# Kernel tuning notes

Hardware: AMD Instinct MI355X
Metric: run time of the kernel (lower is better)

Reference implementation:

```python
import jax, jax.numpy as jnp
import numpy as np

B, N, VF, EF, DV, DE, LN = 64, 64, 32, 16, 128, 128, 4
EPS_INNER = 128.0  # BatchNorm1d(MAX_N, internal_d_vert): 2nd positional arg is eps (faithful to source bug)
EPS_BN = 1e-5


def gev_layer(v_in, e_in, evW, evb, eW, eb, vW, vb, relu=True):
    act = jax.nn.relu if relu else (lambda x: x)
    ev = v_in @ evW + evb                                   # [B,N,De]
    # outer_v_sum: ev.unsqueeze(1) + ev.unsqueeze(2) -> [B,N,N,De]
    e_out = act(e_in @ eW + eb + ev[:, None, :, :] + ev[:, :, None, :])
    per_v_e = e_out.sum(axis=1)                             # sum-aggregate over dim 1
    v_out = act(jnp.concatenate([per_v_e, v_in], axis=-1) @ vW + vb)
    return v_out, e_out


def bn_flat(v, g, b):
    # BatchNorm1d(N*VF) on [B, N*VF] in training mode (biased var)
    x = v.reshape(-1, N * VF)
    mu = x.mean(axis=0)
    var = x.var(axis=0)
    x = (x - mu) * jax.lax.rsqrt(var + EPS_BN) * g + b
    return x.reshape(-1, N, VF)


def bn_inner(v, g, b):
    # BatchNorm1d(MAX_N, eps=128) on [B, N, D]: channels are the N axis, stats over (B, D)
    mu = v.mean(axis=(0, 2), keepdims=True)
    var = v.var(axis=(0, 2), keepdims=True)
    return (v - mu) * jax.lax.rsqrt(var + EPS_INNER) * g[None, :, None] + b[None, :, None]


def setup_inputs() -> dict:
    key = jax.random.key(0)
    ks = jax.random.split(key, 24)
    s = 0.01  # force_lin_init with init_noise=0.01, biases zero
    nrm = lambda k, shp: jax.random.normal(k, shp, dtype=jnp.float32) * s
    inp = {
        "v": jax.random.normal(ks[0], (B, N, VF), dtype=jnp.float32),
        "e": jax.random.normal(ks[1], (B, N, N, EF), dtype=jnp.float32),
        "bn_in_g": jnp.ones((N * VF,), jnp.float32),
        "bn_in_b": jnp.zeros((N * VF,), jnp.float32),
        "g1_evW": nrm(ks[2], (VF, DE)), "g1_evb": jnp.zeros((DE,), jnp.float32),
        "g1_eW": nrm(ks[3], (EF, DE)), "g1_eb": jnp.zeros((DE,), jnp.float32),
        "g1_vW": nrm(ks[4], (VF + DE, DV)), "g1_vb": jnp.zeros((DV,), jnp.float32),
        "inn_evW": nrm(ks[5], (LN, DV, DE)), "inn_evb": jnp.zeros((LN, DE), jnp.float32),
        "inn_eW": nrm(ks[6], (LN, DE, DE)), "inn_eb": jnp.zeros((LN, DE), jnp.float32),
        "inn_vW": nrm(ks[7], (LN, DV + DE, DV)), "inn_vb": jnp.zeros((LN, DV), jnp.float32),
        "bn_g": jnp.ones((LN, N), jnp.float32),
        "bn_b": jnp.zeros((LN, N), jnp.float32),
        "g3_evW": nrm(ks[8], (DV, 1)), "g3_evb": jnp.zeros((1,), jnp.float32),
        "g3_eW": nrm(ks[9], (DE, 1)), "g3_eb": jnp.zeros((1,), jnp.float32),
        "g3_vW": nrm(ks[10], (DV + 1, 1)), "g3_vb": jnp.zeros((1,), jnp.float32),
    }
    return inp


def reference(v, e, bn_in_g, bn_in_b, g1_evW, g1_evb, g1_eW, g1_eb, g1_vW, g1_vb,
              inn_evW, inn_evb, inn_eW, inn_eb, inn_vW, inn_vb, bn_g, bn_b,
              g3_evW, g3_evb, g3_eW, g3_eb, g3_vW, g3_vb):
    v = bn_flat(v, bn_in_g, bn_in_b)
    v, e = gev_layer(v, e, g1_evW, g1_evb, g1_eW, g1_eb, g1_vW, g1_vb)
    for i in range(LN):
        v_next, e_next = gev_layer(v, e, inn_evW[i], inn_evb[i], inn_eW[i], inn_eb[i], inn_vW[i], inn_vb[i])
        v = v_next + v  # resnet
        e = e_next + e
        v = bn_inner(v, bn_g[i], bn_b[i])
    v, e = gev_layer(v, e, g3_evW, g3_evb, g3_eW, g3_eb, g3_vW, g3_vb, relu=False)
    return v, e
```

## Files before the change

### kernel.cpp

```cpp
#include <hip/hip_runtime.h>
#include <hip/hip_bf16.h>


typedef __bf16 bf16_t;
typedef __bf16 bf16x8 __attribute__((ext_vector_type(8)));
typedef __bf16 bf16x4 __attribute__((ext_vector_type(4)));
typedef float f32x4 __attribute__((ext_vector_type(4)));

__device__ __forceinline__ void bar_lgkm() {
  asm volatile("s_waitcnt lgkmcnt(0)\n\ts_barrier" ::: "memory");
}

__global__ __launch_bounds__(256) void k_prep(const float* __restrict__ vin,
    const float* __restrict__ g, const float* __restrict__ bt,
    const float* __restrict__ eW, float* __restrict__ v0,
    bf16_t* __restrict__ Wt, float* __restrict__ stats) {
  __shared__ float red[8][32][2];
  __shared__ float scb[32], shb[32];
  const int blk = blockIdx.x, tid = threadIdx.x;
  if (blk < 64) {
    const int chq = tid & 31, bq = tid >> 5;
    const int ch = blk * 32 + chq;
    float s = 0.f, s2 = 0.f;
#pragma unroll
    for (int t = 0; t < 8; ++t) {
      float x = vin[(bq * 8 + t) * 2048 + ch];
      s += x; s2 += x * x;
    }
    red[bq][chq][0] = s;
    red[bq][chq][1] = s2;
    __syncthreads();
    if (tid < 32) {
      float S = 0.f, S2 = 0.f;
#pragma unroll
      for (int q = 0; q < 8; ++q) { S += red[q][tid][0]; S2 += red[q][tid][1]; }
      float mu = S * (1.f / 64.f);
      float var = S2 * (1.f / 64.f) - mu * mu;
      float sc = rsqrtf(var + 1e-5f) * g[blk * 32 + tid];
      scb[tid] = sc;
      shb[tid] = bt[blk * 32 + tid] - mu * sc;
    }
    __syncthreads();
    const float sc = scb[chq], sh = shb[chq];
#pragma unroll
    for (int t = 0; t < 8; ++t) {
      int b = bq * 8 + t;
      v0[b * 2048 + ch] = vin[b * 2048 + ch] * sc + sh;
    }
  } else if (blk < 320) {
    int idx = (blk - 64) * 256 + tid;
    int l = idx >> 14, r = idx & 16383, n = r >> 7, k = r & 127;
    Wt[idx] = (bf16_t)eW[(l << 14) + (k << 7) + n];
  } else {
    for (int i = tid; i < 512; i += 256) stats[i] = 0.f;
  }
}

template <int K>
__global__ __launch_bounds__(256) void k_ev(const float* __restrict__ v_in,
    const float* __restrict__ W, const float* __restrict__ bias,
    float* __restrict__ out) {
  __shared__ float rows_s[8][K];
  const int r0 = blockIdx.x * 8;
  const int tid = threadIdx.x;
  const int c = tid & 127, h = tid >> 7;
  for (int idx = tid; idx < 8 * K; idx += 256) {
    int rr = idx / K, kk = idx % K;
    rows_s[rr][kk] = v_in[(r0 + rr) * K + kk];
  }
  __syncthreads();
  float acc[4];
  const float bv = bias[c];
#pragma unroll
  for (int r = 0; r < 4; ++r) acc[r] = bv;
  for (int k4 = 0; k4 < K; k4 += 4) {
    float w0 = W[(k4 + 0) * 128 + c], w1 = W[(k4 + 1) * 128 + c];
    float w2 = W[(k4 + 2) * 128 + c], w3 = W[(k4 + 3) * 128 + c];
#pragma unroll
    for (int r = 0; r < 4; ++r) {
      float4 x = *(const float4*)&rows_s[h * 4 + r][k4];
      acc[r] += x.x * w0 + x.y * w1 + x.z * w2 + x.w * w3;
    }
  }
#pragma unroll
  for (int r = 0; r < 4; ++r) out[(r0 + h * 4 + r) * 128 + c] = acc[r];
}

__global__ __launch_bounds__(256) void k_evbn(float* __restrict__ v,
    const float* __restrict__ stats, const float* __restrict__ g,
    const float* __restrict__ bt, const float* __restrict__ W,
    const float* __restrict__ bias, float* __restrict__ out) {
  __shared__ float rows_s[8][128];
  const int r0 = blockIdx.x * 8;
  const int tid = threadIdx.x;
  const int c = tid & 127, h = tid >> 7;
#pragma unroll
  for (int u = 0; u < 4; ++u) {
    int idx = u * 256 + tid;
    int rr = idx >> 7, k = idx & 127;
    int n = (r0 + rr) & 63;
    float mu = stats[n] * (1.f / 8192.f);
    float var = stats[64 + n] * (1.f / 8192.f) - mu * mu;
    float sc = rsqrtf(var + 128.f) * g[n];
    float x = (v[(r0 + rr) * 128 + k] - mu) * sc + bt[n];
    rows_s[rr][k] = x;
    v[(r0 + rr) * 128 + k] = x;
  }
  __syncthreads();
  float acc[4];
  const float bv = bias[c];
#pragma unroll
  for (int r = 0; r < 4; ++r) acc[r] = bv;
  for (int k4 = 0; k4 < 128; k4 += 4) {
    float w0 = W[(k4 + 0) * 128 + c], w1 = W[(k4 + 1) * 128 + c];
    float w2 = W[(k4 + 2) * 128 + c], w3 = W[(k4 + 3) * 128 + c];
#pragma unroll
    for (int r = 0; r < 4; ++r) {
      float4 x = *(const float4*)&rows_s[h * 4 + r][k4];
      acc[r] += x.x * w0 + x.y * w1 + x.z * w2 + x.w * w3;
    }
  }
#pragma unroll
  for (int r = 0; r < 4; ++r) out[(r0 + h * 4 + r) * 128 + c] = acc[r];
}

__global__ __launch_bounds__(256) void k_edge_g1(const float* __restrict__ e0,
    const float* __restrict__ eW, const float* __restrict__ eb,
    const float* __restrict__ ev, bf16_t* __restrict__ e_ws,
    float* __restrict__ pve) {
  __shared__ bf16_t A0s[2][64][40];
  __shared__ bf16_t Os[2][64][136];
  const int b = blockIdx.x >> 5, j0 = (blockIdx.x & 31) * 2;
  const int tid = threadIdx.x;
  const int lane = tid & 63, w = tid >> 6;
  const int quad = lane >> 4, l16 = lane & 15;
#pragma unroll
  for (int t = 0; t < 2; ++t) {
    int idx = tid + t * 256;
    int row = idx >> 3, off = (idx & 7) * 4;
    int jc = off >> 4, k = off & 15;
    f32x4 x = *(const f32x4*)&e0[((b * 64 + row) * 64 + j0) * 16 + off];
    bf16x4 y;
#pragma unroll
    for (int r = 0; r < 4; ++r) y[r] = (bf16_t)x[r];
    *(bf16x4*)&A0s[jc][row][k] = y;
    bf16x4 z = {(bf16_t)0.f, (bf16_t)0.f, (bf16_t)0.f, (bf16_t)0.f};
    *(bf16x4*)&A0s[jc][row][16 + k] = z;
  }
  const int c0[2] = {w * 32 + quad * 4, w * 32 + 16 + quad * 4};
  bf16x8 wf[2];
#pragma unroll
  for (int nt = 0; nt < 2; ++nt) {
    const int c = w * 32 + nt * 16 + l16;
#pragma unroll
    for (int jj = 0; jj < 8; ++jj)
      wf[nt][jj] = (quad < 2) ? (bf16_t)eW[(quad * 8 + jj) * 128 + c] : (bf16_t)0.f;
  }
  f32x4 acc[2][4][2];
  {
    f32x4 ebv[2], evj[2][2], evi[4][2];
#pragma unroll
    for (int nt = 0; nt < 2; ++nt) {
      ebv[nt] = *(const f32x4*)&eb[c0[nt]];
#pragma unroll
      for (int jc = 0; jc < 2; ++jc)
        evj[jc][nt] = *(const f32x4*)&ev[(b * 64 + j0 + jc) * 128 + c0[nt]];
#pragma unroll
      for (int mt = 0; mt < 4; ++mt)
        evi[mt][nt] = *(const f32x4*)&ev[(b * 64 + mt * 16 + l16) * 128 + c0[nt]];
    }
#pragma unroll
    for (int jc = 0; jc < 2; ++jc)
#pragma unroll
      for (int mt = 0; mt < 4; ++mt)
#pragma unroll
        for (int nt = 0; nt < 2; ++nt)
          acc[jc][mt][nt] = ebv[nt] + evj[jc][nt] + evi[mt][nt];
  }
  __syncthreads();
#pragma unroll
  for (int jc = 0; jc < 2; ++jc) {
#pragma unroll
    for (int mt = 0; mt < 4; ++mt) {
      bf16x8 ef = *(const bf16x8*)&A0s[jc][mt * 16 + l16][quad * 8];
#pragma unroll
      for (int nt = 0; nt < 2; ++nt)
        acc[jc][mt][nt] = __builtin_amdgcn_mfma_f32_16x16x32_bf16(wf[nt], ef, acc[jc][mt][nt], 0, 0, 0);
    }
  }
#pragma unroll
  for (int jc = 0; jc < 2; ++jc) {
#pragma unroll
    for (int nt = 0; nt < 2; ++nt) {
      f32x4 ps = {0.f, 0.f, 0.f, 0.f};
#pragma unroll
      for (int mt = 0; mt < 4; ++mt) {
        const int i = mt * 16 + l16;
        bf16x4 outv;
#pragma unroll
        for (int r = 0; r < 4; ++r) {
          float vv = fmaxf(acc[jc][mt][nt][r], 0.f);
          ps[r] += vv;
          outv[r] = (bf16_t)vv;
        }
        *(bf16x4*)&Os[jc][i][c0[nt]] = outv;
      }
#pragma unroll
      for (int m = 1; m <= 8; m <<= 1) {
#pragma unroll
        for (int r = 0; r < 4; ++r) ps[r] += __shfl_xor(ps[r], m);
      }
      if (l16 == 0) *(f32x4*)&pve[(b * 64 + j0 + jc) * 128 + c0[nt]] = ps;
    }
  }
  __syncthreads();
  {
    bf16_t* ebase = &e_ws[((size_t)(b * 64 + j0) * 64) * 128];
#pragma unroll
    for (int t = 0; t < 8; ++t) {
      int idx = tid + t * 256;
      *(int4*)&ebase[idx * 8] =
          *(const int4*)&Os[idx >> 10][(idx >> 4) & 63][(idx & 15) * 8];
    }
  }
}

__global__ __launch_bounds__(256) void k_vg1_ev(const float* __restrict__ pve,
    const float* __restrict__ v0, const float* __restrict__ vW,
    const float* __restrict__ vb, const float* __restrict__ evW,
    const float* __restrict__ evb, float* __restrict__ v, float* __restrict__ ev) {
  __shared__ float in_s[8][160];
  __shared__ float vr[8][128];
  const int r0 = blockIdx.x * 8;
  const int tid = threadIdx.x;
  const int c = tid & 127, h = tid >> 7;
#pragma unroll
  for (int u = 0; u < 4; ++u) {
    int idx = u * 256 + tid;
    int rr = idx >> 7, k = idx & 127;
    in_s[rr][k] = pve[(r0 + rr) * 128 + k];
  }
  {
    int rr = tid >> 5, k = tid & 31;
    in_s[rr][128 + k] = v0[(r0 + rr) * 32 + k];
  }
  __syncthreads();
  float acc[4];
  const float bv = vb[c];
#pragma unroll
  for (int r = 0; r < 4; ++r) acc[r] = bv;
  for (int k4 = 0; k4 < 160; k4 += 4) {
    float w0 = vW[(k4 + 0) * 128 + c], w1 = vW[(k4 + 1) * 128 + c];
    float w2 = vW[(k4 + 2) * 128 + c], w3 = vW[(k4 + 3) * 128 + c];
#pragma unroll
    for (int r = 0; r < 4; ++r) {
      float4 x = *(const float4*)&in_s[h * 4 + r][k4];
      acc[r] += x.x * w0 + x.y * w1 + x.z * w2 + x.w * w3;
    }
  }
#pragma unroll
  for (int r = 0; r < 4; ++r) {
    float val = fmaxf(acc[r], 0.f);
    vr[h * 4 + r][c] = val;
    v[(r0 + h * 4 + r) * 128 + c] = val;
  }
  __syncthreads();
  float acc2[4];
  const float bv2 = evb[c];
#pragma unroll
  for (int r = 0; r < 4; ++r) acc2[r] = bv2;
  for (int k4 = 0; k4 < 128; k4 += 4) {
    float w0 = evW[(k4 + 0) * 128 + c], w1 = evW[(k4 + 1) * 128 + c];
    float w2 = evW[(k4 + 2) * 128 + c], w3 = evW[(k4 + 3) * 128 + c];
#pragma unroll
    for (int r = 0; r < 4; ++r) {
      float4 x = *(const float4*)&vr[h * 4 + r][k4];
      acc2[r] += x.x * w0 + x.y * w1 + x.z * w2 + x.w * w3;
    }
  }
#pragma unroll
  for (int r = 0; r < 4; ++r) ev[(r0 + h * 4 + r) * 128 + c] = acc2[r];
}

template <bool LAST>
__global__ __launch_bounds__(256) void k_edge_inner(bf16_t* __restrict__ e_ws,
    const bf16_t* __restrict__ Wt, const float* __restrict__ eb,
    const float* __restrict__ ev, float* __restrict__ pve,
    const float* __restrict__ eW3, float* __restrict__ edt) {
  __shared__ bf16_t As[2][64][136];
  __shared__ float W3s[128];
  const int b = blockIdx.x >> 5, j0 = (blockIdx.x & 31) * 2;
  const int tid = threadIdx.x;
  const int lane = tid & 63, w = tid >> 6;
  const int quad = lane >> 4, l16 = lane & 15;
  bf16_t* ebase = &e_ws[((size_t)(b * 64 + j0) * 64) * 128];
  int4 stg[8];
#pragma unroll
  for (int t = 0; t < 8; ++t) {
    int idx = tid + t * 256;
    stg[t] = *(const int4*)&ebase[idx * 8];
  }
  if (LAST) {
    if (tid < 128) W3s[tid] = eW3[tid];
  }
  bf16x8 wf[2][4];
#pragma unroll
  for (int nt = 0; nt < 2; ++nt)
#pragma unroll
    for (int ks = 0; ks < 4; ++ks)
      wf[nt][ks] = *(const bf16x8*)&Wt[(w * 32 + nt * 16 + l16) * 128 + ks * 32 + quad * 8];
  const int c0[2] = {w * 32 + quad * 4, w * 32 + 16 + quad * 4};
  f32x4 acc[2][4][2];
  {
    f32x4 ebv[2], evj[2][2], evi[4][2];
#pragma unroll
    for (int nt = 0; nt < 2; ++nt) {
      ebv[nt] = *(const f32x4*)&eb[c0[nt]];
#pragma unroll
      for (int jc = 0; jc < 2; ++jc)
        evj[jc][nt] = *(const f32x4*)&ev[(b * 64 + j0 + jc) * 128 + c0[nt]];
#pragma unroll
      for (int mt = 0; mt < 4; ++mt)
        evi[mt][nt] = *(const f32x4*)&ev[(b * 64 + mt * 16 + l16) * 128 + c0[nt]];
    }
#pragma unroll
    for (int jc = 0; jc < 2; ++jc)
#pragma unroll
      for (int mt = 0; mt < 4; ++mt)
#pragma unroll
        for (int nt = 0; nt < 2; ++nt)
          acc[jc][mt][nt] = ebv[nt] + evj[jc][nt] + evi[mt][nt];
  }
#pragma unroll
  for (int t = 0; t < 8; ++t) {
    int idx = tid + t * 256;
    *(int4*)&As[idx >> 10][(idx >> 4) & 63][(idx & 15) * 8] = stg[t];
  }
  bar_lgkm();
#pragma unroll
  for (int ks = 0; ks < 4; ++ks) {
    bf16x8 ef[2][4];
#pragma unroll
    for (int jc = 0; jc < 2; ++jc)
#pragma unroll
      for (int mt = 0; mt < 4; ++mt)
        ef[jc][mt] = *(const bf16x8*)&As[jc][mt * 16 + l16][ks * 32 + quad * 8];
#pragma unroll
    for (int jc = 0; jc < 2; ++jc)
#pragma unroll
      for (int mt = 0; mt < 4; ++mt)
#pragma unroll
        for (int nt = 0; nt < 2; ++nt)
          acc[jc][mt][nt] = __builtin_amdgcn_mfma_f32_16x16x32_bf16(wf[nt][ks], ef[jc][mt], acc[jc][mt][nt], 0, 0, 0);
  }
  if (!LAST) {
#pragma unroll
    for (int jc = 0; jc < 2; ++jc) {
#pragma unroll
      for (int nt = 0; nt < 2; ++nt) {
        f32x4 ps = {0.f, 0.f, 0.f, 0.f};
#pragma unroll
        for (int mt = 0; mt < 4; ++mt) {
          const int i = mt * 16 + l16;
          bf16x4 eo = *(const bf16x4*)&As[jc][i][c0[nt]];
          bf16x4 outv;
#pragma unroll
          for (int r = 0; r < 4; ++r) {
            float vv = fmaxf(acc[jc][mt][nt][r], 0.f);
            ps[r] += vv;
            outv[r] = (bf16_t)(vv + (float)eo[r]);
          }
          *(bf16x4*)&ebase[jc * 8192 + i * 128 + c0[nt]] = outv;
        }
#pragma unroll
        for (int m = 1; m <= 8; m <<= 1) {
#pragma unroll
          for (int r = 0; r < 4; ++r) ps[r] += __shfl_xor(ps[r], m);
        }
        if (l16 == 0) *(f32x4*)&pve[(b * 64 + j0 + jc) * 128 + c0[nt]] = ps;
      }
    }
  } else {
    bar_lgkm();
#pragma unroll
    for (int jc = 0; jc < 2; ++jc) {
#pragma unroll
      for (int nt = 0; nt < 2; ++nt) {
        f32x4 ps = {0.f, 0.f, 0.f, 0.f};
#pragma unroll
        for (int mt = 0; mt < 4; ++mt) {
          const int i = mt * 16 + l16;
          bf16x4 eo = *(const bf16x4*)&As[jc][i][c0[nt]];
          bf16x4 outv;
#pragma unroll
          for (int r = 0; r < 4; ++r) {
            float vv = fmaxf(acc[jc][mt][nt][r], 0.f);
            ps[r] += vv;
            outv[r] = (bf16_t)(vv + (float)eo[r]);
          }
          *(bf16x4*)&As[jc][i][c0[nt]] = outv;
        }
#pragma unroll
        for (int m = 1; m <= 8; m <<= 1) {
#pragma unroll
          for (int r = 0; r < 4; ++r) ps[r] += __shfl_xor(ps[r], m);
        }
        if (l16 == 0) *(f32x4*)&pve[(b * 64 + j0 + jc) * 128 + c0[nt]] = ps;
      }
    }
    bar_lgkm();
    const int i = tid >> 2, q = tid & 3;
#pragma unroll
    for (int jc = 0; jc < 2; ++jc) {
      float d = 0.f;
#pragma unroll
      for (int t = 0; t < 4; ++t) {
        bf16x8 x = *(const bf16x8*)&As[jc][i][q * 32 + t * 8];
#pragma unroll
        for (int u = 0; u < 8; ++u) d += (float)x[u] * W3s[q * 32 + t * 8 + u];
      }
      d += __shfl_xor(d, 1);
      d += __shfl_xor(d, 2);
      if (q == 0) edt[(b * 64 + j0 + jc) * 64 + i] = d;
    }
  }
}

__global__ __launch_bounds__(256) void k_v_inner(const float* __restrict__ pve,
    float* __restrict__ v, const float* __restrict__ vW,
    const float* __restrict__ vb, float* __restrict__ stats) {
  __shared__ float in_s[8][256];
  __shared__ float outs[8][132];
  __shared__ float part[16][2];
  const int r0 = blockIdx.x * 8;
  const int tid = threadIdx.x;
  const int c = tid & 127, h = tid >> 7;
#pragma unroll
  for (int u = 0; u < 4; ++u) {
    int idx = u * 256 + tid;
    int rr = idx >> 7, k = idx & 127;
    in_s[rr][k] = pve[(r0 + rr) * 128 + k];
    in_s[rr][128 + k] = v[(r0 + rr) * 128 + k];
  }
  __syncthreads();
  float acc[4];
  const float bv = vb[c];
#pragma unroll
  for (int r = 0; r < 4; ++r) acc[r] = bv;
  for (int k4 = 0; k4 < 256; k4 += 4) {
    float w0 = vW[(k4 + 0) * 128 + c], w1 = vW[(k4 + 1) * 128 + c];
    float w2 = vW[(k4 + 2) * 128 + c], w3 = vW[(k4 + 3) * 128 + c];
#pragma unroll
    for (int r = 0; r < 4; ++r) {
      float4 x = *(const float4*)&in_s[h * 4 + r][k4];
      acc[r] += x.x * w0 + x.y * w1 + x.z * w2 + x.w * w3;
    }
  }
#pragma unroll
  for (int r = 0; r < 4; ++r) {
    float val = fmaxf(acc[r], 0.f) + in_s[h * 4 + r][128 + c];
    outs[h * 4 + r][c] = val;
    v[(r0 + h * 4 + r) * 128 + c] = val;
  }
  __syncthreads();
  if (tid < 16) {
    int rr = tid >> 1, half = tid & 1;
    float s = 0.f, s2 = 0.f;
    for (int k = 0; k < 64; ++k) {
      float x = outs[rr][half * 64 + k];
      s += x; s2 += x * x;
    }
    part[tid][0] = s;
    part[tid][1] = s2;
  }
  __syncthreads();
  if (tid < 8) {
    int n = (r0 + tid) & 63;
    atomicAdd(&stats[n], part[tid * 2][0] + part[tid * 2 + 1][0]);
    atomicAdd(&stats[64 + n], part[tid * 2][1] + part[tid * 2 + 1][1]);
  }
}

__global__ __launch_bounds__(256) void k_g3(const float* __restrict__ vv,
    const float* __restrict__ stats3, const float* __restrict__ g,
    const float* __restrict__ bt, const float* __restrict__ evW3,
    const float* __restrict__ evb3, const float* __restrict__ eb3,
    const float* __restrict__ edt, const float* __restrict__ vW3,
    const float* __restrict__ vb3, float* __restrict__ out_v,
    float* __restrict__ out_e) {
  __shared__ float vbn[64][132];
  __shared__ float edts[64][68];
  __shared__ float scs[64], shs[64];
  __shared__ float W3e[128];
  __shared__ float vWs[132];
  __shared__ float ev3s[64];
  __shared__ float pj[4][64];
  const int b = blockIdx.x, tid = threadIdx.x;
  if (tid < 64) {
    float mu = stats3[tid] * (1.f / 8192.f);
    float var = stats3[64 + tid] * (1.f / 8192.f) - mu * mu;
    float sc = rsqrtf(var + 128.f) * g[tid];
    scs[tid] = sc;
    shs[tid] = bt[tid] - mu * sc;
  }
  if (tid < 128) W3e[tid] = evW3[tid];
  if (tid < 129) vWs[tid] = vW3[tid];
  __syncthreads();
#pragma unroll
  for (int t = 0; t < 8; ++t) {
    int idx = t * 1024 + tid * 4;
    int row = idx >> 7, cc = idx & 127;
    f32x4 x = *(const f32x4*)&vv[(b * 64 + row) * 128 + cc];
    *(f32x4*)&vbn[row][cc] = x * scs[row] + shs[row];
  }
#pragma unroll
  for (int t = 0; t < 4; ++t) {
    int idx = t * 1024 + tid * 4;
    int j = idx >> 6, i = idx & 63;
    *(f32x4*)&edts[j][i] = *(const f32x4*)&edt[(b * 64 + j) * 64 + i];
  }
  __syncthreads();
  {
    int i = tid >> 2, q = tid & 3;
    float d = 0.f;
#pragma unroll
    for (int u = 0; u < 32; ++u) d += vbn[i][q * 32 + u] * W3e[q * 32 + u];
    d += __shfl_xor(d, 1);
    d += __shfl_xor(d, 2);
    if (q == 0) ev3s[i] = d + evb3[0];
  }
  __syncthreads();
  {
    int q = tid >> 6, j = tid & 63;
    float s = 0.f;
    const float e3 = eb3[0];
    const float evj = ev3s[j];
#pragma unroll
    for (int r = 0; r < 16; ++r) {
      int i = q * 16 + r;
      float val = edts[j][i] + e3 + ev3s[i] + evj;
      out_e[(b * 64 + i) * 64 + j] = val;
      s += val;
    }
    pj[q][j] = s;
  }
  __syncthreads();
  {
    int n = tid >> 2, q = tid & 3;
    float d = 0.f;
#pragma unroll
    for (int u = 0; u < 32; ++u) d += vbn[n][q * 32 + u] * vWs[1 + q * 32 + u];
    d += __shfl_xor(d, 1);
    d += __shfl_xor(d, 2);
    if (q == 0) {
      float p3 = pj[0][n] + pj[1][n] + pj[2][n] + pj[3][n];
      out_v[b * 64 + n] = d + p3 * vWs[0] + vb3[0];
    }
  }
}

extern "C" void kernel_launch(void* const* d_in, const int* in_sizes, int n_in,
                              void* d_out, int out_size, void* d_ws, size_t ws_size,
                              hipStream_t stream) {
  const float* in_v    = (const float*)d_in[0];
  const float* in_e    = (const float*)d_in[1];
  const float* bn_in_g = (const float*)d_in[2];
  const float* bn_in_b = (const float*)d_in[3];
  const float* g1_evW  = (const float*)d_in[4];
  const float* g1_evb  = (const float*)d_in[5];
  const float* g1_eW   = (const float*)d_in[6];
  const float* g1_eb   = (const float*)d_in[7];
  const float* g1_vW   = (const float*)d_in[8];
  const float* g1_vb   = (const float*)d_in[9];
  const float* inn_evW = (const float*)d_in[10];
  const float* inn_evb = (const float*)d_in[11];
  const float* inn_eW  = (const float*)d_in[12];
  const float* inn_eb  = (const float*)d_in[13];
  const float* inn_vW  = (const float*)d_in[14];
  const float* inn_vb  = (const float*)d_in[15];
  const float* bn_g    = (const float*)d_in[16];
  const float* bn_b    = (const float*)d_in[17];
  const float* g3_evW  = (const float*)d_in[18];
  const float* g3_evb  = (const float*)d_in[19];
  const float* g3_eW   = (const float*)d_in[20];
  const float* g3_eb   = (const float*)d_in[21];
  const float* g3_vW   = (const float*)d_in[22];
  const float* g3_vb   = (const float*)d_in[23];

  char* ws = (char*)d_ws;
  bf16_t* e_ws = (bf16_t*)(ws);
  float* v     = (float*)(ws + 67108864);
  float* ev    = (float*)(ws + 69206016);
  float* pve   = (float*)(ws + 71303168);
  float* v0    = (float*)(ws + 73400320);
  bf16_t* Wt   = (bf16_t*)(ws + 73924608);
  float* edt   = (float*)(ws + 74055680);
  float* stats = (float*)(ws + 75104256);

  float* out_v = (float*)d_out;
  float* out_e = (float*)d_out + 4096;

  k_prep<<<321, 256, 0, stream>>>(in_v, bn_in_g, bn_in_b, inn_eW, v0, Wt, stats);

  k_ev<32><<<512, 256, 0, stream>>>(v0, g1_evW, g1_evb, ev);
  k_edge_g1<<<2048, 256, 0, stream>>>(in_e, g1_eW, g1_eb, ev, e_ws, pve);
  k_vg1_ev<<<512, 256, 0, stream>>>(pve, v0, g1_vW, g1_vb, inn_evW, inn_evb, v, ev);

  for (int l = 0; l < 4; ++l) {
    if (l > 0)
      k_evbn<<<512, 256, 0, stream>>>(v, stats + (l - 1) * 128, bn_g + (l - 1) * 64,
                                      bn_b + (l - 1) * 64, inn_evW + l * 16384,
                                      inn_evb + l * 128, ev);
    if (l < 3)
      k_edge_inner<false><<<2048, 256, 0, stream>>>(e_ws, Wt + l * 16384,
          inn_eb + l * 128, ev, pve, g3_eW, edt);
    else
      k_edge_inner<true><<<2048, 256, 0, stream>>>(e_ws, Wt + l * 16384,
          inn_eb + l * 128, ev, pve, g3_eW, edt);
    k_v_inner<<<512, 256, 0, stream>>>(pve, v, inn_vW + l * 32768, inn_vb + l * 128,
                                       stats + l * 128);
  }

  k_g3<<<64, 256, 0, stream>>>(v, stats + 384, bn_g + 192, bn_b + 192,
                               g3_evW, g3_evb, g3_eb, edt, g3_vW, g3_vb,
                               out_v, out_e);
}
```

Measured before the change: 381.6 us.

## Fold inner BatchNorm into edge projection via column sums, drop k_evbn launches

Result: faster. 371.1 us (-2.8%).

```diff
diff --git a/kernel.cpp b/kernel.cpp
--- a/kernel.cpp
+++ b/kernel.cpp
@@ -13,8 +13,9 @@
 
 __global__ __launch_bounds__(256) void k_prep(const float* __restrict__ vin,
     const float* __restrict__ g, const float* __restrict__ bt,
-    const float* __restrict__ eW, float* __restrict__ v0,
-    bf16_t* __restrict__ Wt, float* __restrict__ stats) {
+    const float* __restrict__ eW, const float* __restrict__ evW,
+    float* __restrict__ v0, bf16_t* __restrict__ Wt,
+    float* __restrict__ stats, float* __restrict__ colsum) {
   __shared__ float red[8][32][2];
   __shared__ float scb[32], shb[32];
   const int blk = blockIdx.x, tid = threadIdx.x;
@@ -53,65 +54,34 @@
     Wt[idx] = (bf16_t)eW[(l << 14) + (k << 7) + n];
   } else {
     for (int i = tid; i < 512; i += 256) stats[i] = 0.f;
-  }
-}
-
-template <int K>
-__global__ __launch_bounds__(256) void k_ev(const float* __restrict__ v_in,
+#pragma unroll
+    for (int t = 0; t < 2; ++t) {
+      int idx = tid + t * 256;
+      int l = idx >> 7, c = idx & 127;
+      float s = 0.f;
+      for (int k = 0; k < 128; ++k) s += evW[(l << 14) + (k << 7) + c];
+      colsum[idx] = s;
+    }
+  }
+}
+
+__global__ __launch_bounds__(256) void k_ev32(const float* __restrict__ v_in,
     const float* __restrict__ W, const float* __restrict__ bias,
     float* __restrict__ out) {
-  __shared__ float rows_s[8][K];
+  __shared__ float rows_s[8][32];
   const int r0 = blockIdx.x * 8;
   const int tid = threadIdx.x;
   const int c = tid & 127, h = tid >> 7;
-  for (int idx = tid; idx < 8 * K; idx += 256) {
-    int rr = idx / K, kk = idx % K;
-    rows_s[rr][kk] = v_in[(r0 + rr) * K + kk];
+  {
+    int rr = tid >> 5, kk = tid & 31;
+    rows_s[rr][kk] = v_in[(r0 + rr) * 32 + kk];
   }
   __syncthreads();
   float acc[4];
   const float bv = bias[c];
 #pragma unroll
   for (int r = 0; r < 4; ++r) acc[r] = bv;
-  for (int k4 = 0; k4 < K; k4 += 4) {
-    float w0 = W[(k4 + 0) * 128 + c], w1 = W[(k4 + 1) * 128 + c];
-    float w2 = W[(k4 + 2) * 128 + c], w3 = W[(k4 + 3) * 128 + c];
-#pragma unroll
-    for (int r = 0; r < 4; ++r) {
-      float4 x = *(const float4*)&rows_s[h * 4 + r][k4];
-      acc[r] += x.x * w0 + x.y * w1 + x.z * w2 + x.w * w3;
-    }
-  }
-#pragma unroll
-  for (int r = 0; r < 4; ++r) out[(r0 + h * 4 + r) * 128 + c] = acc[r];
-}
-
-__global__ __launch_bounds__(256) void k_evbn(float* __restrict__ v,
-    const float* __restrict__ stats, const float* __restrict__ g,
-    const float* __restrict__ bt, const float* __restrict__ W,
-    const float* __restrict__ bias, float* __restrict__ out) {
-  __shared__ float rows_s[8][128];
-  const int r0 = blockIdx.x * 8;
-  const int tid = threadIdx.x;
-  const int c = tid & 127, h = tid >> 7;
-#pragma unroll
-  for (int u = 0; u < 4; ++u) {
-    int idx = u * 256 + tid;
-    int rr = idx >> 7, k = idx & 127;
-    int n = (r0 + rr) & 63;
-    float mu = stats[n] * (1.f / 8192.f);
-    float var = stats[64 + n] * (1.f / 8192.f) - mu * mu;
-    float sc = rsqrtf(var + 128.f) * g[n];
-    float x = (v[(r0 + rr) * 128 + k] - mu) * sc + bt[n];
-    rows_s[rr][k] = x;
-    v[(r0 + rr) * 128 + k] = x;
-  }
-  __syncthreads();
-  float acc[4];
-  const float bv = bias[c];
-#pragma unroll
-  for (int r = 0; r < 4; ++r) acc[r] = bv;
-  for (int k4 = 0; k4 < 128; k4 += 4) {
+  for (int k4 = 0; k4 < 32; k4 += 4) {
     float w0 = W[(k4 + 0) * 128 + c], w1 = W[(k4 + 1) * 128 + c];
     float w2 = W[(k4 + 2) * 128 + c], w3 = W[(k4 + 3) * 128 + c];
 #pragma unroll
@@ -228,7 +198,7 @@
 __global__ __launch_bounds__(256) void k_vg1_ev(const float* __restrict__ pve,
     const float* __restrict__ v0, const float* __restrict__ vW,
     const float* __restrict__ vb, const float* __restrict__ evW,
-    const float* __restrict__ evb, float* __restrict__ v, float* __restrict__ ev) {
+    float* __restrict__ v, float* __restrict__ ev) {
   __shared__ float in_s[8][160];
   __shared__ float vr[8][128];
   const int r0 = blockIdx.x * 8;
@@ -265,10 +235,7 @@
     v[(r0 + h * 4 + r) * 128 + c] = val;
   }
   __syncthreads();
-  float acc2[4];
-  const float bv2 = evb[c];
-#pragma unroll
-  for (int r = 0; r < 4; ++r) acc2[r] = bv2;
+  float acc2[4] = {0.f, 0.f, 0.f, 0.f};
   for (int k4 = 0; k4 < 128; k4 += 4) {
     float w0 = evW[(k4 + 0) * 128 + c], w1 = evW[(k4 + 1) * 128 + c];
     float w2 = evW[(k4 + 2) * 128 + c], w3 = evW[(k4 + 3) * 128 + c];
@@ -285,15 +252,31 @@
 template <bool LAST>
 __global__ __launch_bounds__(256) void k_edge_inner(bf16_t* __restrict__ e_ws,
     const bf16_t* __restrict__ Wt, const float* __restrict__ eb,
-    const float* __restrict__ ev, float* __restrict__ pve,
-    const float* __restrict__ eW3, float* __restrict__ edt) {
+    const float* __restrict__ evb, const float* __restrict__ rawev,
+    const float* __restrict__ colsum, const float* __restrict__ stats_prev,
+    const float* __restrict__ g_prev, const float* __restrict__ bt_prev,
+    float* __restrict__ pve, const float* __restrict__ eW3,
+    float* __restrict__ edt) {
   __shared__ bf16_t As[2][64][136];
   __shared__ float W3s[128];
+  __shared__ float scs[64], shs[64];
   const int b = blockIdx.x >> 5, j0 = (blockIdx.x & 31) * 2;
   const int tid = threadIdx.x;
   const int lane = tid & 63, w = tid >> 6;
   const int quad = lane >> 4, l16 = lane & 15;
   bf16_t* ebase = &e_ws[((size_t)(b * 64 + j0) * 64) * 128];
+  if (tid < 64) {
+    if (stats_prev) {
+      float mu = stats_prev[tid] * (1.f / 8192.f);
+      float var = stats_prev[64 + tid] * (1.f / 8192.f) - mu * mu;
+      float sc = rsqrtf(var + 128.f) * g_prev[tid];
+      scs[tid] = sc;
+      shs[tid] = bt_prev[tid] - mu * sc;
+    } else {
+      scs[tid] = 1.f;
+      shs[tid] = 0.f;
+    }
+  }
   int4 stg[8];
 #pragma unroll
   for (int t = 0; t < 8; ++t) {
@@ -310,26 +293,19 @@
     for (int ks = 0; ks < 4; ++ks)
       wf[nt][ks] = *(const bf16x8*)&Wt[(w * 32 + nt * 16 + l16) * 128 + ks * 32 + quad * 8];
   const int c0[2] = {w * 32 + quad * 4, w * 32 + 16 + quad * 4};
-  f32x4 acc[2][4][2];
-  {
-    f32x4 ebv[2], evj[2][2], evi[4][2];
-#pragma unroll
-    for (int nt = 0; nt < 2; ++nt) {
-      ebv[nt] = *(const f32x4*)&eb[c0[nt]];
-#pragma unroll
-      for (int jc = 0; jc < 2; ++jc)
-        evj[jc][nt] = *(const f32x4*)&ev[(b * 64 + j0 + jc) * 128 + c0[nt]];
-#pragma unroll
-      for (int mt = 0; mt < 4; ++mt)
-        evi[mt][nt] = *(const f32x4*)&ev[(b * 64 + mt * 16 + l16) * 128 + c0[nt]];
-    }
+  f32x4 basev[2], cs[2], evj[2][2], evi[4][2];
+#pragma unroll
+  for (int nt = 0; nt < 2; ++nt) {
+    f32x4 e1 = *(const f32x4*)&eb[c0[nt]];
+    f32x4 e2 = *(const f32x4*)&evb[c0[nt]];
+    basev[nt] = e1 + 2.f * e2;
+    cs[nt] = *(const f32x4*)&colsum[c0[nt]];
 #pragma unroll
     for (int jc = 0; jc < 2; ++jc)
-#pragma unroll
-      for (int mt = 0; mt < 4; ++mt)
-#pragma unroll
-        for (int nt = 0; nt < 2; ++nt)
-          acc[jc][mt][nt] = ebv[nt] + evj[jc][nt] + evi[mt][nt];
+      evj[jc][nt] = *(const f32x4*)&rawev[(b * 64 + j0 + jc) * 128 + c0[nt]];
+#pragma unroll
+    for (int mt = 0; mt < 4; ++mt)
+      evi[mt][nt] = *(const f32x4*)&rawev[(b * 64 + mt * 16 + l16) * 128 + c0[nt]];
   }
 #pragma unroll
   for (int t = 0; t < 8; ++t) {
@@ -337,6 +313,24 @@
     *(int4*)&As[idx >> 10][(idx >> 4) & 63][(idx & 15) * 8] = stg[t];
   }
   bar_lgkm();
+  f32x4 acc[2][4][2];
+  {
+    float scj[2], shj[2];
+#pragma unroll
+    for (int jc = 0; jc < 2; ++jc) { scj[jc] = scs[j0 + jc]; shj[jc] = shs[j0 + jc]; }
+#pragma unroll
+    for (int mt = 0; mt < 4; ++mt) {
+      const int i = mt * 16 + l16;
+      const float sci = scs[i], shi = shs[i];
+#pragma unroll
+      for (int jc = 0; jc < 2; ++jc) {
+        const float shsum = shi + shj[jc];
+#pragma unroll
+        for (int nt = 0; nt < 2; ++nt)
+          acc[jc][mt][nt] = basev[nt] + shsum * cs[nt] + scj[jc] * evj[jc][nt] + sci * evi[mt][nt];
+      }
+    }
+  }
 #pragma unroll
   for (int ks = 0; ks < 4; ++ks) {
     bf16x8 ef[2][4];
@@ -353,62 +347,42 @@
         for (int nt = 0; nt < 2; ++nt)
           acc[jc][mt][nt] = __builtin_amdgcn_mfma_f32_16x16x32_bf16(wf[nt][ks], ef[jc][mt], acc[jc][mt][nt], 0, 0, 0);
   }
+  bar_lgkm();
+#pragma unroll
+  for (int jc = 0; jc < 2; ++jc) {
+#pragma unroll
+    for (int nt = 0; nt < 2; ++nt) {
+      f32x4 ps = {0.f, 0.f, 0.f, 0.f};
+#pragma unroll
+      for (int mt = 0; mt < 4; ++mt) {
+        const int i = mt * 16 + l16;
+        bf16x4 eo = *(const bf16x4*)&As[jc][i][c0[nt]];
+        bf16x4 outv;
+#pragma unroll
+        for (int r = 0; r < 4; ++r) {
+          float vv = fmaxf(acc[jc][mt][nt][r], 0.f);
+          ps[r] += vv;
+          outv[r] = (bf16_t)(vv + (float)eo[r]);
+        }
+        *(bf16x4*)&As[jc][i][c0[nt]] = outv;
+      }
+#pragma unroll
+      for (int m = 1; m <= 8; m <<= 1) {
+#pragma unroll
+        for (int r = 0; r < 4; ++r) ps[r] += __shfl_xor(ps[r], m);
+      }
+      if (l16 == 0) *(f32x4*)&pve[(b * 64 + j0 + jc) * 128 + c0[nt]] = ps;
+    }
+  }
+  bar_lgkm();
   if (!LAST) {
 #pragma unroll
-    for (int jc = 0; jc < 2; ++jc) {
-#pragma unroll
-      for (int nt = 0; nt < 2; ++nt) {
-        f32x4 ps = {0.f, 0.f, 0.f, 0.f};
-#pragma unroll
-        for (int mt = 0; mt < 4; ++mt) {
-          const int i = mt * 16 + l16;
-          bf16x4 eo = *(const bf16x4*)&As[jc][i][c0[nt]];
-          bf16x4 outv;
-#pragma unroll
-          for (int r = 0; r < 4; ++r) {
-            float vv = fmaxf(acc[jc][mt][nt][r], 0.f);
-            ps[r] += vv;
-            outv[r] = (bf16_t)(vv + (float)eo[r]);
-          }
-          *(bf16x4*)&ebase[jc * 8192 + i * 128 + c0[nt]] = outv;
-        }
-#pragma unroll
-        for (int m = 1; m <= 8; m <<= 1) {
-#pragma unroll
-          for (int r = 0; r < 4; ++r) ps[r] += __shfl_xor(ps[r], m);
-        }
-        if (l16 == 0) *(f32x4*)&pve[(b * 64 + j0 + jc) * 128 + c0[nt]] = ps;
-      }
+    for (int t = 0; t < 8; ++t) {
+      int idx = tid + t * 256;
+      *(int4*)&ebase[idx * 8] =
+          *(const int4*)&As[idx >> 10][(idx >> 4) & 63][(idx & 15) * 8];
     }
   } else {
-    bar_lgkm();
-#pragma unroll
-    for (int jc = 0; jc < 2; ++jc) {
-#pragma unroll
-      for (int nt = 0; nt < 2; ++nt) {
-        f32x4 ps = {0.f, 0.f, 0.f, 0.f};
-#pragma unroll
-        for (int mt = 0; mt < 4; ++mt) {
-          const int i = mt * 16 + l16;
-          bf16x4 eo = *(const bf16x4*)&As[jc][i][c0[nt]];
-          bf16x4 outv;
-#pragma unroll
-          for (int r = 0; r < 4; ++r) {
-            float vv = fmaxf(acc[jc][mt][nt][r], 0.f);
-            ps[r] += vv;
-            outv[r] = (bf16_t)(vv + (float)eo[r]);
-          }
-          *(bf16x4*)&As[jc][i][c0[nt]] = outv;
-        }
-#pragma unroll
-        for (int m = 1; m <= 8; m <<= 1) {
-#pragma unroll
-          for (int r = 0; r < 4; ++r) ps[r] += __shfl_xor(ps[r], m);
-        }
-        if (l16 == 0) *(f32x4*)&pve[(b * 64 + j0 + jc) * 128 + c0[nt]] = ps;
-      }
-    }
-    bar_lgkm();
     const int i = tid >> 2, q = tid & 3;
 #pragma unroll
     for (int jc = 0; jc < 2; ++jc) {
@@ -428,19 +402,37 @@
 
 __global__ __launch_bounds__(256) void k_v_inner(const float* __restrict__ pve,
     float* __restrict__ v, const float* __restrict__ vW,
-    const float* __restrict__ vb, float* __restrict__ stats) {
+    const float* __restrict__ vb, float* __restrict__ stats,
+    const float* __restrict__ stats_prev, const float* __restrict__ g_prev,
+    const float* __restrict__ bt_prev, const float* __restrict__ evW_next,
+    float* __restrict__ rawev) {
   __shared__ float in_s[8][256];
   __shared__ float outs[8][132];
   __shared__ float part[16][2];
+  __shared__ float scb[8], shb[8];
   const int r0 = blockIdx.x * 8;
   const int tid = threadIdx.x;
   const int c = tid & 127, h = tid >> 7;
+  if (tid < 8) {
+    int n = (r0 + tid) & 63;
+    if (stats_prev) {
+      float mu = stats_prev[n] * (1.f / 8192.f);
+      float var = stats_prev[64 + n] * (1.f / 8192.f) - mu * mu;
+      float sc = rsqrtf(var + 128.f) * g_prev[n];
+      scb[tid] = sc;
+      shb[tid] = bt_prev[n] - mu * sc;
+    } else {
+      scb[tid] = 1.f;
+      shb[tid] = 0.f;
+    }
+  }
+  __syncthreads();
 #pragma unroll
   for (int u = 0; u < 4; ++u) {
     int idx = u * 256 + tid;
     int rr = idx >> 7, k = idx & 127;
     in_s[rr][k] = pve[(r0 + rr) * 128 + k];
-    in_s[rr][128 + k] = v[(r0 + rr) * 128 + k];
+    in_s[rr][128 + k] = v[(r0 + rr) * 128 + k] * scb[rr] + shb[rr];
   }
   __syncthreads();
   float acc[4];
@@ -463,6 +455,20 @@
     v[(r0 + h * 4 + r) * 128 + c] = val;
   }
   __syncthreads();
+  if (evW_next) {
+    float acc2[4] = {0.f, 0.f, 0.f, 0.f};
+    for (int k4 = 0; k4 < 128; k4 += 4) {
+      float w0 = evW_next[(k4 + 0) * 128 + c], w1 = evW_next[(k4 + 1) * 128 + c];
+      float w2 = evW_next[(k4 + 2) * 128 + c], w3 = evW_next[(k4 + 3) * 128 + c];
+#pragma unroll
+      for (int r = 0; r < 4; ++r) {
+        float4 x = *(const float4*)&outs[h * 4 + r][k4];
+        acc2[r] += x.x * w0 + x.y * w1 + x.z * w2 + x.w * w3;
+      }
+    }
+#pragma unroll
+    for (int r = 0; r < 4; ++r) rawev[(r0 + h * 4 + r) * 128 + c] = acc2[r];
+  }
   if (tid < 16) {
     int rr = tid >> 1, half = tid & 1;
     float s = 0.f, s2 = 0.f;
@@ -588,37 +594,43 @@
   const float* g3_vb   = (const float*)d_in[23];
 
   char* ws = (char*)d_ws;
-  bf16_t* e_ws = (bf16_t*)(ws);
-  float* v     = (float*)(ws + 67108864);
-  float* ev    = (float*)(ws + 69206016);
-  float* pve   = (float*)(ws + 71303168);
-  float* v0    = (float*)(ws + 73400320);
-  bf16_t* Wt   = (bf16_t*)(ws + 73924608);
-  float* edt   = (float*)(ws + 74055680);
-  float* stats = (float*)(ws + 75104256);
+  bf16_t* e_ws  = (bf16_t*)(ws);
+  float* v      = (float*)(ws + 67108864);
+  float* ev     = (float*)(ws + 69206016);
+  float* pve    = (float*)(ws + 71303168);
+  float* ev_g1  = (float*)(ws + 73400320);
+  float* v0     = (float*)(ws + 75497472);
+  bf16_t* Wt    = (bf16_t*)(ws + 76021760);
+  float* edt    = (float*)(ws + 76152832);
+  float* stats  = (float*)(ws + 77201408);
+  float* colsum = (float*)(ws + 77203456);
 
   float* out_v = (float*)d_out;
   float* out_e = (float*)d_out + 4096;
 
-  k_prep<<<321, 256, 0, stream>>>(in_v, bn_in_g, bn_in_b, inn_eW, v0, Wt, stats);
-
-  k_ev<32><<<512, 256, 0, stream>>>(v0, g1_evW, g1_evb, ev);
-  k_edge_g1<<<2048, 256, 0, stream>>>(in_e, g1_eW, g1_eb, ev, e_ws, pve);
-  k_vg1_ev<<<512, 256, 0, stream>>>(pve, v0, g1_vW, g1_vb, inn_evW, inn_evb, v, ev);
+  k_prep<<<321, 256, 0, stream>>>(in_v, bn_in_g, bn_in_b, inn_eW, inn_evW,
+                                  v0, Wt, stats, colsum);
+
+  k_ev32<<<512, 256, 0, stream>>>(v0, g1_evW, g1_evb, ev_g1);
+  k_edge_g1<<<2048, 256, 0, stream>>>(in_e, g1_eW, g1_eb, ev_g1, e_ws, pve);
+  k_vg1_ev<<<512, 256, 0, stream>>>(pve, v0, g1_vW, g1_vb, inn_evW, v, ev);
 
   for (int l = 0; l < 4; ++l) {
-    if (l > 0)
-      k_evbn<<<512, 256, 0, stream>>>(v, stats + (l - 1) * 128, bn_g + (l - 1) * 64,
-                                      bn_b + (l - 1) * 64, inn_evW + l * 16384,
-                                      inn_evb + l * 128, ev);
+    const float* sp = (l > 0) ? stats + (l - 1) * 128 : nullptr;
+    const float* gp = bn_g + (l > 0 ? (l - 1) * 64 : 0);
+    const float* bp = bn_b + (l > 0 ? (l - 1) * 64 : 0);
     if (l < 3)
       k_edge_inner<false><<<2048, 256, 0, stream>>>(e_ws, Wt + l * 16384,
-          inn_eb + l * 128, ev, pve, g3_eW, edt);
+          inn_eb + l * 128, inn_evb + l * 128, ev, colsum + l * 128,
+          sp, gp, bp, pve, g3_eW, edt);
     else
       k_edge_inner<true><<<2048, 256, 0, stream>>>(e_ws, Wt + l * 16384,
-          inn_eb + l * 128, ev, pve, g3_eW, edt);
+          inn_eb + l * 128, inn_evb + l * 128, ev, colsum + l * 128,
+          sp, gp, bp, pve, g3_eW, edt);
     k_v_inner<<<512, 256, 0, stream>>>(pve, v, inn_vW + l * 32768, inn_vb + l * 128,
-                                       stats + l * 128);
+                                       stats + l * 128, sp, gp, bp,
+                                       (l < 3) ? inn_evW + (l + 1) * 16384 : nullptr,
+                                       ev);
   }
 
   k_g3<<<64, 256, 0, stream>>>(v, stats + 384, bn_g + 192, bn_b + 192,
```
